# Performance work log

Hardware: AMD Instinct MI355X
Metric: run time of the kernel (lower is better)

## Reference

```python
import jax, jax.numpy as jnp
import numpy as np

N_NODES = 50000
N_EDGES = 800000
HIDDEN = 128
N_LAYERS = 3
MAX_Z = 1000
N_GRAPHS = 512
LN_EPS = 1e-5


def setup_inputs() -> dict:
    key = jax.random.key(0)
    ks = jax.random.split(key, 16)
    s = 0.05
    inp = {
        "z": jax.random.randint(ks[0], (N_NODES,), 0, MAX_Z),
        "edge_index": jax.random.randint(ks[1], (2, N_EDGES), 0, N_NODES),
        "batch": jnp.sort(jax.random.randint(ks[2], (N_NODES,), 0, N_GRAPHS)),
        "z_table": jax.random.normal(ks[3], (MAX_Z, HIDDEN), jnp.float32) * s,
        "W1": jax.random.normal(ks[4], (N_LAYERS, HIDDEN, HIDDEN), jnp.float32) * s,
        "b1": jnp.zeros((N_LAYERS, HIDDEN), jnp.float32),
        "W2": jax.random.normal(ks[5], (N_LAYERS, HIDDEN, HIDDEN), jnp.float32) * s,
        "b2": jnp.zeros((N_LAYERS, HIDDEN), jnp.float32),
        "ln_g": jnp.ones((N_LAYERS, HIDDEN), jnp.float32),
        "ln_b": jnp.zeros((N_LAYERS, HIDDEN), jnp.float32),
        "lin1_W": jax.random.normal(ks[6], (N_LAYERS * HIDDEN, HIDDEN), jnp.float32) * s,
        "lin1_b": jnp.zeros((HIDDEN,), jnp.float32),
        "lin2_W": jax.random.normal(ks[7], (HIDDEN, 1), jnp.float32) * s,
        "lin2_b": jnp.zeros((1,), jnp.float32),
    }
    return inp


def _layernorm(h, g, b):
    mu = jnp.mean(h, axis=-1, keepdims=True)
    var = jnp.mean((h - mu) ** 2, axis=-1, keepdims=True)
    return g * (h - mu) * jax.lax.rsqrt(var + LN_EPS) + b


def _gin_conv(x, src, dst, W1, b1, W2, b2, g, b):
    # sum-aggregate neighbor features, eps = 0 (train_eps=False)
    agg = jax.ops.segment_sum(x[src], dst, num_segments=N_NODES)
    h = x + agg
    h = jax.nn.relu(h @ W1 + b1)
    h = jax.nn.relu(h @ W2 + b2)
    return _layernorm(h, g, b)


def reference(z, edge_index, batch, z_table, W1, b1, W2, b2, ln_g, ln_b,
              lin1_W, lin1_b, lin2_W, lin2_b):
    src, dst = edge_index[0], edge_index[1]
    x = z_table[z]  # [N, H] z embedding (z is 1-D so no sum over dim 1)
    xs = []
    for l in range(N_LAYERS):
        x = _gin_conv(x, src, dst, W1[l], b1[l], W2[l], b2[l], ln_g[l], ln_b[l])
        xs.append(x)
    xcat = jnp.concatenate(xs, axis=1)  # JK concat [N, L*H]
    # global mean pool over graphs
    sums = jax.ops.segment_sum(xcat, batch, num_segments=N_GRAPHS)
    cnts = jax.ops.segment_sum(jnp.ones((N_NODES, 1), xcat.dtype), batch,
                               num_segments=N_GRAPHS)
    pooled = sums / jnp.maximum(cnts, 1.0)
    h = jax.nn.relu(pooled @ lin1_W + lin1_b)
    # dropout is identity in eval mode
    return h @ lin2_W + lin2_b  # [N_GRAPHS, 1]
```

## Files before the change

kernel.cpp:

```cpp
#include <hip/hip_runtime.h>
#include <hip/hip_bf16.h>

#define NN 50000
#define NE 800000
#define HD 128
#define NL 3
#define NG 512
#define LN_EPS 1e-5f
#define NXCD 8
#define NPX 6250

typedef unsigned short u16;
typedef unsigned int u32;
typedef __attribute__((ext_vector_type(8))) short short8;
typedef __attribute__((ext_vector_type(4))) float f32x4;

__device__ __forceinline__ u16 f2bf(float f){
  u32 x = __float_as_uint(f);
  u32 r = (x + 0x7fffu + ((x >> 16) & 1u)) >> 16;
  return (u16)r;
}
__device__ __forceinline__ float blo(u32 u){ return __uint_as_float(u << 16); }
__device__ __forceinline__ float bhi(u32 u){ return __uint_as_float(u & 0xffff0000u); }
__device__ __forceinline__ u32 pk2(float a, float b){ return (u32)f2bf(a) | ((u32)f2bf(b) << 16); }

__device__ __forceinline__ int lower_bound_dev(const int* a, int n, int v){
  int lo = 0, hi = n;
  while (lo < hi){ int m = (lo + hi) >> 1; if (a[m] < v) lo = m + 1; else hi = m; }
  return lo;
}

__global__ __launch_bounds__(256) void k_prep_w(const float* __restrict__ W1,
    const float* __restrict__ W2, u16* __restrict__ Wt){
  int t = blockIdx.x * 256 + threadIdx.x;
  if (t >= 6 * 128 * 128) return;
  int w = t >> 14, r = t & 16383, n = r >> 7, k = r & 127;
  int l = w >> 1;
  const float* Ws = (w & 1) ? (W2 + l * 16384) : (W1 + l * 16384);
  Wt[t] = f2bf(Ws[k * 128 + n]);
}

__global__ __launch_bounds__(256) void k_embed(const int* __restrict__ z,
    const float* __restrict__ tab, u16* __restrict__ xb){
  int gt = blockIdx.x * 256 + threadIdx.x;
  int node = gt >> 5, q = gt & 31;
  float4 v = *reinterpret_cast<const float4*>(tab + (size_t)z[node] * 128 + q * 4);
  uint2 p = { pk2(v.x, v.y), pk2(v.z, v.w) };
  *reinterpret_cast<uint2*>(xb + (size_t)node * 128 + q * 4) = p;
}

__global__ __launch_bounds__(256) void k_count(const int* __restrict__ dst,
    int* __restrict__ deg){
  int xcd = blockIdx.x & 7;
  int grp = blockIdx.x >> 3;
  int nlo = xcd * NPX, nhi = nlo + NPX;
  for (int e = grp * 256 + threadIdx.x; e < NE; e += 128 * 256){
    int d = dst[e];
    if (d >= nlo && d < nhi) atomicAdd(&deg[d], 1);
  }
}

__global__ __launch_bounds__(256) void k_scan1(const int* __restrict__ deg,
    int* __restrict__ part, int* __restrict__ bsum){
  int i = blockIdx.x * 256 + threadIdx.x;
  int v = (i < NN) ? deg[i] : 0;
  int lane = threadIdx.x & 63, wave = threadIdx.x >> 6;
  int s = v;
  for (int off = 1; off < 64; off <<= 1){ int n = __shfl_up(s, off); if (lane >= off) s += n; }
  __shared__ int wsums[4];
  if (lane == 63) wsums[wave] = s;
  __syncthreads();
  int add = 0;
  for (int w = 0; w < wave; ++w) add += wsums[w];
  int incl = s + add;
  if (i < NN) part[i] = incl - v;
  if (threadIdx.x == 255) bsum[blockIdx.x] = incl;
}

__global__ __launch_bounds__(256) void k_scan2(int* __restrict__ bsum, int nb){
  int tid = threadIdx.x;
  int v = (tid < nb) ? bsum[tid] : 0;
  int lane = tid & 63, wave = tid >> 6;
  int s = v;
  for (int off = 1; off < 64; off <<= 1){ int n = __shfl_up(s, off); if (lane >= off) s += n; }
  __shared__ int wsums[4];
  if (lane == 63) wsums[wave] = s;
  __syncthreads();
  int add = 0;
  for (int w = 0; w < wave; ++w) add += wsums[w];
  int incl = s + add;
  if (tid < nb) bsum[tid] = incl - v;
}

__global__ __launch_bounds__(256) void k_scan3(const int* __restrict__ part,
    const int* __restrict__ bsum, int* __restrict__ rowptr, int* __restrict__ cursor){
  int i = blockIdx.x * 256 + threadIdx.x;
  if (i < NN){ int r = part[i] + bsum[blockIdx.x]; rowptr[i] = r; cursor[i] = r; }
  if (i == 0) rowptr[NN] = NE;
}

__global__ __launch_bounds__(256) void k_fill(const int* __restrict__ src,
    const int* __restrict__ dst, int* __restrict__ cursor, u16* __restrict__ col){
  int xcd = blockIdx.x & 7;
  int grp = blockIdx.x >> 3;
  int nlo = xcd * NPX, nhi = nlo + NPX;
  for (int e = grp * 256 + threadIdx.x; e < NE; e += 128 * 256){
    int d = dst[e];
    if (d >= nlo && d < nhi){
      int p = atomicAdd(&cursor[d], 1);
      col[p] = (u16)src[e];
    }
  }
}

__global__ __launch_bounds__(256) void k_gather(const int* __restrict__ rowptr,
    const u16* __restrict__ col, const u16* __restrict__ xb, u16* __restrict__ hb){
  int wave = threadIdx.x >> 6, lane = threadIdx.x & 63;
  int node = blockIdx.x * 4 + wave;
  int q = lane >> 4, l4 = lane & 15;
  float a[8] = {0.f,0.f,0.f,0.f,0.f,0.f,0.f,0.f};
  float b[8] = {0.f,0.f,0.f,0.f,0.f,0.f,0.f,0.f};
  if (q == 0){
    uint4 s = *reinterpret_cast<const uint4*>(xb + (size_t)node * 128 + l4 * 8);
    a[0] = blo(s.x); a[1] = bhi(s.x); a[2] = blo(s.y); a[3] = bhi(s.y);
    a[4] = blo(s.z); a[5] = bhi(s.z); a[6] = blo(s.w); a[7] = bhi(s.w);
  }
  int lo = rowptr[node], hi = rowptr[node + 1];
  int e = lo + q;
  for (; e + 12 < hi; e += 16){
    int c0 = col[e], c1 = col[e + 4], c2 = col[e + 8], c3 = col[e + 12];
    uint4 v0 = *reinterpret_cast<const uint4*>(xb + (size_t)c0 * 128 + l4 * 8);
    uint4 v1 = *reinterpret_cast<const uint4*>(xb + (size_t)c1 * 128 + l4 * 8);
    uint4 v2 = *reinterpret_cast<const uint4*>(xb + (size_t)c2 * 128 + l4 * 8);
    uint4 v3 = *reinterpret_cast<const uint4*>(xb + (size_t)c3 * 128 + l4 * 8);
    a[0] += blo(v0.x); a[1] += bhi(v0.x); a[2] += blo(v0.y); a[3] += bhi(v0.y);
    a[4] += blo(v0.z); a[5] += bhi(v0.z); a[6] += blo(v0.w); a[7] += bhi(v0.w);
    b[0] += blo(v1.x); b[1] += bhi(v1.x); b[2] += blo(v1.y); b[3] += bhi(v1.y);
    b[4] += blo(v1.z); b[5] += bhi(v1.z); b[6] += blo(v1.w); b[7] += bhi(v1.w);
    a[0] += blo(v2.x); a[1] += bhi(v2.x); a[2] += blo(v2.y); a[3] += bhi(v2.y);
    a[4] += blo(v2.z); a[5] += bhi(v2.z); a[6] += blo(v2.w); a[7] += bhi(v2.w);
    b[0] += blo(v3.x); b[1] += bhi(v3.x); b[2] += blo(v3.y); b[3] += bhi(v3.y);
    b[4] += blo(v3.z); b[5] += bhi(v3.z); b[6] += blo(v3.w); b[7] += bhi(v3.w);
  }
  for (; e < hi; e += 4){
    int c0 = col[e];
    uint4 v0 = *reinterpret_cast<const uint4*>(xb + (size_t)c0 * 128 + l4 * 8);
    a[0] += blo(v0.x); a[1] += bhi(v0.x); a[2] += blo(v0.y); a[3] += bhi(v0.y);
    a[4] += blo(v0.z); a[5] += bhi(v0.z); a[6] += blo(v0.w); a[7] += bhi(v0.w);
  }
  #pragma unroll
  for (int j = 0; j < 8; ++j){
    a[j] += b[j];
    a[j] += __shfl_xor(a[j], 16);
    a[j] += __shfl_xor(a[j], 32);
  }
  if (q == 0){
    uint4 p = { pk2(a[0], a[1]), pk2(a[2], a[3]), pk2(a[4], a[5]), pk2(a[6], a[7]) };
    *reinterpret_cast<uint4*>(hb + (size_t)node * 128 + l4 * 8) = p;
  }
}

__global__ __launch_bounds__(256) void k_layer(const u16* __restrict__ A,
    const u16* __restrict__ Wt1, const u16* __restrict__ Wt2,
    const float* __restrict__ bias1, const float* __restrict__ bias2,
    const float* __restrict__ lng, const float* __restrict__ lnb,
    u16* __restrict__ Cout, const int* __restrict__ batch,
    float* __restrict__ pooled, int lsl){
  __shared__ u16 As[128 * 128];
  __shared__ int sb[128];
  int tid = threadIdx.x;
  int rb = blockIdx.x * 128;

  #pragma unroll
  for (int i = 0; i < 8; ++i){
    int u = tid + i * 256;
    int row = u >> 4, k8 = u & 15;
    int grow = rb + row;
    uint4 v = {0u, 0u, 0u, 0u};
    if (grow < NN) v = *reinterpret_cast<const uint4*>(A + (size_t)grow * 128 + k8 * 8);
    *reinterpret_cast<uint4*>(&As[row * 128 + (k8 ^ (row & 15)) * 8]) = v;
  }
  if (tid < 128){
    int grow = rb + tid;
    sb[tid] = (grow < NN) ? batch[grow] : -1;
  }
  __syncthreads();

  int wave = tid >> 6, lane = tid & 63;
  int lrow = lane & 15, kgrp = lane >> 4;
  f32x4 acc[2][8];
  #pragma unroll
  for (int rt = 0; rt < 2; ++rt)
    #pragma unroll
    for (int nt = 0; nt < 8; ++nt) acc[rt][nt] = (f32x4){0.f, 0.f, 0.f, 0.f};

  #pragma unroll
  for (int ks = 0; ks < 4; ++ks){
    int ch = ks * 4 + kgrp;
    short8 a0 = *reinterpret_cast<const short8*>(&As[(wave * 32 + lrow) * 128 + (ch ^ lrow) * 8]);
    short8 a1 = *reinterpret_cast<const short8*>(&As[(wave * 32 + 16 + lrow) * 128 + (ch ^ lrow) * 8]);
    #pragma unroll
    for (int nt = 0; nt < 8; ++nt){
      short8 b = *reinterpret_cast<const short8*>(Wt1 + (nt * 16 + lrow) * 128 + ch * 8);
      acc[0][nt] = __builtin_amdgcn_mfma_f32_16x16x32_bf16(a0, b, acc[0][nt], 0, 0, 0);
      acc[1][nt] = __builtin_amdgcn_mfma_f32_16x16x32_bf16(a1, b, acc[1][nt], 0, 0, 0);
    }
  }

  #pragma unroll
  for (int nt = 0; nt < 8; ++nt){
    float bv = __ldg(bias1 + nt * 16 + lrow);
    #pragma unroll
    for (int rt = 0; rt < 2; ++rt)
      #pragma unroll
      for (int j = 0; j < 4; ++j)
        acc[rt][nt][j] = fmaxf(acc[rt][nt][j] + bv, 0.f);
  }

  __syncthreads();
  #pragma unroll
  for (int rt = 0; rt < 2; ++rt)
    #pragma unroll
    for (int j = 0; j < 4; ++j){
      int row = wave * 32 + rt * 16 + kgrp * 4 + j;
      #pragma unroll
      for (int nt = 0; nt < 8; ++nt){
        int col = nt * 16 + lrow;
        int ch = (col >> 3) ^ (row & 15);
        As[row * 128 + ch * 8 + (col & 7)] = f2bf(acc[rt][nt][j]);
      }
    }
  __syncthreads();

  #pragma unroll
  for (int rt = 0; rt < 2; ++rt)
    #pragma unroll
    for (int nt = 0; nt < 8; ++nt) acc[rt][nt] = (f32x4){0.f, 0.f, 0.f, 0.f};

  #pragma unroll
  for (int ks = 0; ks < 4; ++ks){
    int ch = ks * 4 + kgrp;
    short8 a0 = *reinterpret_cast<const short8*>(&As[(wave * 32 + lrow) * 128 + (ch ^ lrow) * 8]);
    short8 a1 = *reinterpret_cast<const short8*>(&As[(wave * 32 + 16 + lrow) * 128 + (ch ^ lrow) * 8]);
    #pragma unroll
    for (int nt = 0; nt < 8; ++nt){
      short8 b = *reinterpret_cast<const short8*>(Wt2 + (nt * 16 + lrow) * 128 + ch * 8);
      acc[0][nt] = __builtin_amdgcn_mfma_f32_16x16x32_bf16(a0, b, acc[0][nt], 0, 0, 0);
      acc[1][nt] = __builtin_amdgcn_mfma_f32_16x16x32_bf16(a1, b, acc[1][nt], 0, 0, 0);
    }
  }

  float gv[8], lbv[8];
  #pragma unroll
  for (int nt = 0; nt < 8; ++nt){
    int gcol = nt * 16 + lrow;
    float bv = __ldg(bias2 + gcol);
    gv[nt] = __ldg(lng + gcol); lbv[nt] = __ldg(lnb + gcol);
    #pragma unroll
    for (int rt = 0; rt < 2; ++rt)
      #pragma unroll
      for (int j = 0; j < 4; ++j)
        acc[rt][nt][j] = fmaxf(acc[rt][nt][j] + bv, 0.f);
  }
  #pragma unroll
  for (int rt = 0; rt < 2; ++rt)
    #pragma unroll
    for (int j = 0; j < 4; ++j){
      float s = 0.f, sq = 0.f;
      #pragma unroll
      for (int nt = 0; nt < 8; ++nt){ float v = acc[rt][nt][j]; s += v; sq += v * v; }
      #pragma unroll
      for (int off = 1; off < 16; off <<= 1){
        s += __shfl_xor(s, off); sq += __shfl_xor(sq, off);
      }
      float mu = s * (1.f / 128.f);
      float var = sq * (1.f / 128.f) - mu * mu;
      float rstd = rsqrtf(var + LN_EPS);
      #pragma unroll
      for (int nt = 0; nt < 8; ++nt)
        acc[rt][nt][j] = gv[nt] * (acc[rt][nt][j] - mu) * rstd + lbv[nt];
    }

  #pragma unroll
  for (int rt = 0; rt < 2; ++rt){
    int rbase = rb + wave * 32 + rt * 16 + kgrp * 4;
    #pragma unroll
    for (int nt = 0; nt < 8; ++nt){
      int gcol = nt * 16 + lrow;
      #pragma unroll
      for (int j = 0; j < 4; ++j){
        int grow = rbase + j;
        if (grow < NN) Cout[(size_t)grow * 128 + gcol] = f2bf(acc[rt][nt][j]);
      }
    }
  }

  __syncthreads();
  #pragma unroll
  for (int rt = 0; rt < 2; ++rt)
    #pragma unroll
    for (int j = 0; j < 4; ++j){
      int row = wave * 32 + rt * 16 + kgrp * 4 + j;
      #pragma unroll
      for (int nt = 0; nt < 8; ++nt){
        int col = nt * 16 + lrow;
        int ch = (col >> 3) ^ (row & 15);
        As[row * 128 + ch * 8 + (col & 7)] = f2bf(acc[rt][nt][j]);
      }
    }
  __syncthreads();
  int f = tid & 127, half = tid >> 7;
  int cur = -1; float sum = 0.f;
  for (int r = half * 64; r < half * 64 + 64; ++r){
    int g = sb[r];
    if (g != cur){
      if (cur >= 0) atomicAdd(&pooled[(size_t)cur * 384 + lsl * 128 + f], sum);
      cur = g; sum = 0.f;
    }
    if (g >= 0){
      int ch = (f >> 3) ^ (r & 15);
      sum += blo((u32)As[r * 128 + ch * 8 + (f & 7)]);
    }
  }
  if (cur >= 0) atomicAdd(&pooled[(size_t)cur * 384 + lsl * 128 + f], sum);
}

__global__ __launch_bounds__(128) void k_final(const float* __restrict__ pooled,
    const int* __restrict__ batch, const float* __restrict__ W1,
    const float* __restrict__ b1, const float* __restrict__ W2,
    const float* __restrict__ b2, float* __restrict__ out){
  int g = blockIdx.x, f = threadIdx.x;
  int lo = lower_bound_dev(batch, NN, g);
  int hi = lower_bound_dev(batch, NN, g + 1);
  float scale = 1.f / fmaxf((float)(hi - lo), 1.f);
  __shared__ float p[384];
  for (int k = f; k < 384; k += 128) p[k] = pooled[(size_t)g * 384 + k] * scale;
  __syncthreads();
  float acc = __ldg(b1 + f);
  for (int k = 0; k < 384; ++k) acc += p[k] * __ldg(W1 + k * 128 + f);
  float hval = fmaxf(acc, 0.f);
  float v = hval * __ldg(W2 + f);
  for (int off = 32; off; off >>= 1) v += __shfl_xor(v, off);
  __shared__ float red[2];
  int lane = f & 63, wave = f >> 6;
  if (lane == 0) red[wave] = v;
  __syncthreads();
  if (f == 0) out[g] = red[0] + red[1] + __ldg(b2);
}

extern "C" void kernel_launch(void* const* d_in, const int* in_sizes, int n_in,
                              void* d_out, int out_size, void* d_ws, size_t ws_size,
                              hipStream_t stream){
  const int*   z     = (const int*)d_in[0];
  const int*   ei    = (const int*)d_in[1];
  const int*   batch = (const int*)d_in[2];
  const float* ztab  = (const float*)d_in[3];
  const float* W1    = (const float*)d_in[4];
  const float* b1    = (const float*)d_in[5];
  const float* W2    = (const float*)d_in[6];
  const float* b2    = (const float*)d_in[7];
  const float* lng   = (const float*)d_in[8];
  const float* lnb   = (const float*)d_in[9];
  const float* l1W   = (const float*)d_in[10];
  const float* l1b   = (const float*)d_in[11];
  const float* l2W   = (const float*)d_in[12];
  const float* l2b   = (const float*)d_in[13];
  float* out = (float*)d_out;

  char* wsb = (char*)d_ws;
  size_t off = 0;
  auto alloc = [&](size_t bytes){ void* p = wsb + off; off += (bytes + 255) & ~(size_t)255; return p; };
  u16*   xbf    = (u16*)alloc((size_t)NN * 128 * 2);
  u16*   hbf    = (u16*)alloc((size_t)NN * 128 * 2);
  u16*   Wt     = (u16*)alloc((size_t)6 * 128 * 128 * 2);
  int*   deg    = (int*)alloc((size_t)NN * 4);
  float* pooled = (float*)alloc((size_t)NG * 384 * 4);
  int*   part   = (int*)alloc((size_t)NN * 4);
  int*   bsum   = (int*)alloc((size_t)256 * 4);
  int*   rowptr = (int*)alloc((size_t)(NN + 1) * 4);
  int*   cursor = (int*)alloc((size_t)NN * 4);
  u16*   col    = (u16*)alloc((size_t)NE * 2);

  const int* srcv = ei;
  const int* dstv = ei + NE;

  size_t zero_bytes = ((size_t)NN * 4 + 255 & ~(size_t)255) + (size_t)NG * 384 * 4;
  hipMemsetAsync(deg, 0, zero_bytes, stream);
  k_prep_w<<<(6 * 128 * 128 + 255) / 256, 256, 0, stream>>>(W1, W2, Wt);
  k_embed<<<NN * 32 / 256, 256, 0, stream>>>(z, ztab, xbf);
  k_count<<<1024, 256, 0, stream>>>(dstv, deg);
  int nb = (NN + 255) / 256;
  k_scan1<<<nb, 256, 0, stream>>>(deg, part, bsum);
  k_scan2<<<1, 256, 0, stream>>>(bsum, nb);
  k_scan3<<<nb, 256, 0, stream>>>(part, bsum, rowptr, cursor);
  k_fill<<<1024, 256, 0, stream>>>(srcv, dstv, cursor, col);

  int gb = (NN + 127) / 128;
  for (int l = 0; l < NL; ++l){
    k_gather<<<NN / 4, 256, 0, stream>>>(rowptr, col, xbf, hbf);
    k_layer<<<gb, 256, 0, stream>>>(hbf,
        Wt + (size_t)(l * 2 + 0) * 16384, Wt + (size_t)(l * 2 + 1) * 16384,
        b1 + l * 128, b2 + l * 128, lng + l * 128, lnb + l * 128, xbf,
        batch, pooled, l);
  }
  k_final<<<NG, 128, 0, stream>>>(pooled, batch, l1W, l1b, l2W, l2b, out);
}
```

Before: 448.1 us.

## Halve k_layer row tile, drop intermediate syncs, coalesce output via LDS

After: 419.3 us. 1.07x faster.

```diff
diff --git a/kernel.cpp b/kernel.cpp
--- a/kernel.cpp
+++ b/kernel.cpp
@@ -166,13 +166,13 @@
     const float* __restrict__ lng, const float* __restrict__ lnb,
     u16* __restrict__ Cout, const int* __restrict__ batch,
     float* __restrict__ pooled, int lsl){
-  __shared__ u16 As[128 * 128];
-  __shared__ int sb[128];
+  __shared__ u16 As[64 * 128];
+  __shared__ int sb[64];
   int tid = threadIdx.x;
-  int rb = blockIdx.x * 128;
-
-  #pragma unroll
-  for (int i = 0; i < 8; ++i){
+  int rb = blockIdx.x * 64;
+
+  #pragma unroll
+  for (int i = 0; i < 4; ++i){
     int u = tid + i * 256;
     int row = u >> 4, k8 = u & 15;
     int grow = rb + row;
@@ -180,7 +180,7 @@
     if (grow < NN) v = *reinterpret_cast<const uint4*>(A + (size_t)grow * 128 + k8 * 8);
     *reinterpret_cast<uint4*>(&As[row * 128 + (k8 ^ (row & 15)) * 8]) = v;
   }
-  if (tid < 128){
+  if (tid < 64){
     int grow = rb + tid;
     sb[tid] = (grow < NN) ? batch[grow] : -1;
   }
@@ -188,65 +188,44 @@
 
   int wave = tid >> 6, lane = tid & 63;
   int lrow = lane & 15, kgrp = lane >> 4;
-  f32x4 acc[2][8];
-  #pragma unroll
-  for (int rt = 0; rt < 2; ++rt)
-    #pragma unroll
-    for (int nt = 0; nt < 8; ++nt) acc[rt][nt] = (f32x4){0.f, 0.f, 0.f, 0.f};
-
+  int wr = wave * 16;
+  f32x4 acc[8];
+
+  #pragma unroll
+  for (int nt = 0; nt < 8; ++nt) acc[nt] = (f32x4){0.f, 0.f, 0.f, 0.f};
   #pragma unroll
   for (int ks = 0; ks < 4; ++ks){
     int ch = ks * 4 + kgrp;
-    short8 a0 = *reinterpret_cast<const short8*>(&As[(wave * 32 + lrow) * 128 + (ch ^ lrow) * 8]);
-    short8 a1 = *reinterpret_cast<const short8*>(&As[(wave * 32 + 16 + lrow) * 128 + (ch ^ lrow) * 8]);
+    short8 a0 = *reinterpret_cast<const short8*>(&As[(wr + lrow) * 128 + (ch ^ lrow) * 8]);
     #pragma unroll
     for (int nt = 0; nt < 8; ++nt){
       short8 b = *reinterpret_cast<const short8*>(Wt1 + (nt * 16 + lrow) * 128 + ch * 8);
-      acc[0][nt] = __builtin_amdgcn_mfma_f32_16x16x32_bf16(a0, b, acc[0][nt], 0, 0, 0);
-      acc[1][nt] = __builtin_amdgcn_mfma_f32_16x16x32_bf16(a1, b, acc[1][nt], 0, 0, 0);
-    }
-  }
-
+      acc[nt] = __builtin_amdgcn_mfma_f32_16x16x32_bf16(a0, b, acc[nt], 0, 0, 0);
+    }
+  }
   #pragma unroll
   for (int nt = 0; nt < 8; ++nt){
     float bv = __ldg(bias1 + nt * 16 + lrow);
     #pragma unroll
-    for (int rt = 0; rt < 2; ++rt)
-      #pragma unroll
-      for (int j = 0; j < 4; ++j)
-        acc[rt][nt][j] = fmaxf(acc[rt][nt][j] + bv, 0.f);
-  }
-
-  __syncthreads();
-  #pragma unroll
-  for (int rt = 0; rt < 2; ++rt)
-    #pragma unroll
     for (int j = 0; j < 4; ++j){
-      int row = wave * 32 + rt * 16 + kgrp * 4 + j;
-      #pragma unroll
-      for (int nt = 0; nt < 8; ++nt){
-        int col = nt * 16 + lrow;
-        int ch = (col >> 3) ^ (row & 15);
-        As[row * 128 + ch * 8 + (col & 7)] = f2bf(acc[rt][nt][j]);
-      }
-    }
-  __syncthreads();
-
-  #pragma unroll
-  for (int rt = 0; rt < 2; ++rt)
-    #pragma unroll
-    for (int nt = 0; nt < 8; ++nt) acc[rt][nt] = (f32x4){0.f, 0.f, 0.f, 0.f};
-
+      float v = fmaxf(acc[nt][j] + bv, 0.f);
+      int row = wr + kgrp * 4 + j;
+      int colc = nt * 16 + lrow;
+      int ch = (colc >> 3) ^ (row & 15);
+      As[row * 128 + ch * 8 + (colc & 7)] = f2bf(v);
+    }
+  }
+
+  #pragma unroll
+  for (int nt = 0; nt < 8; ++nt) acc[nt] = (f32x4){0.f, 0.f, 0.f, 0.f};
   #pragma unroll
   for (int ks = 0; ks < 4; ++ks){
     int ch = ks * 4 + kgrp;
-    short8 a0 = *reinterpret_cast<const short8*>(&As[(wave * 32 + lrow) * 128 + (ch ^ lrow) * 8]);
-    short8 a1 = *reinterpret_cast<const short8*>(&As[(wave * 32 + 16 + lrow) * 128 + (ch ^ lrow) * 8]);
+    short8 a0 = *reinterpret_cast<const short8*>(&As[(wr + lrow) * 128 + (ch ^ lrow) * 8]);
     #pragma unroll
     for (int nt = 0; nt < 8; ++nt){
       short8 b = *reinterpret_cast<const short8*>(Wt2 + (nt * 16 + lrow) * 128 + ch * 8);
-      acc[0][nt] = __builtin_amdgcn_mfma_f32_16x16x32_bf16(a0, b, acc[0][nt], 0, 0, 0);
-      acc[1][nt] = __builtin_amdgcn_mfma_f32_16x16x32_bf16(a1, b, acc[1][nt], 0, 0, 0);
+      acc[nt] = __builtin_amdgcn_mfma_f32_16x16x32_bf16(a0, b, acc[nt], 0, 0, 0);
     }
   }
 
@@ -257,69 +236,66 @@
     float bv = __ldg(bias2 + gcol);
     gv[nt] = __ldg(lng + gcol); lbv[nt] = __ldg(lnb + gcol);
     #pragma unroll
-    for (int rt = 0; rt < 2; ++rt)
-      #pragma unroll
-      for (int j = 0; j < 4; ++j)
-        acc[rt][nt][j] = fmaxf(acc[rt][nt][j] + bv, 0.f);
-  }
-  #pragma unroll
-  for (int rt = 0; rt < 2; ++rt)
+    for (int j = 0; j < 4; ++j)
+      acc[nt][j] = fmaxf(acc[nt][j] + bv, 0.f);
+  }
+  #pragma unroll
+  for (int j = 0; j < 4; ++j){
+    float s = 0.f, sq = 0.f;
+    #pragma unroll
+    for (int nt = 0; nt < 8; ++nt){ float v = acc[nt][j]; s += v; sq += v * v; }
+    #pragma unroll
+    for (int off = 1; off < 16; off <<= 1){
+      s += __shfl_xor(s, off); sq += __shfl_xor(sq, off);
+    }
+    float mu = s * (1.f / 128.f);
+    float var = sq * (1.f / 128.f) - mu * mu;
+    float rstd = rsqrtf(var + LN_EPS);
+    #pragma unroll
+    for (int nt = 0; nt < 8; ++nt)
+      acc[nt][j] = gv[nt] * (acc[nt][j] - mu) * rstd + lbv[nt];
+  }
+
+  #pragma unroll
+  for (int nt = 0; nt < 8; ++nt)
     #pragma unroll
     for (int j = 0; j < 4; ++j){
-      float s = 0.f, sq = 0.f;
-      #pragma unroll
-      for (int nt = 0; nt < 8; ++nt){ float v = acc[rt][nt][j]; s += v; sq += v * v; }
-      #pragma unroll
-      for (int off = 1; off < 16; off <<= 1){
-        s += __shfl_xor(s, off); sq += __shfl_xor(sq, off);
-      }
-      float mu = s * (1.f / 128.f);
-      float var = sq * (1.f / 128.f) - mu * mu;
-      float rstd = rsqrtf(var + LN_EPS);
-      #pragma unroll
-      for (int nt = 0; nt < 8; ++nt)
-        acc[rt][nt][j] = gv[nt] * (acc[rt][nt][j] - mu) * rstd + lbv[nt];
-    }
-
-  #pragma unroll
-  for (int rt = 0; rt < 2; ++rt){
-    int rbase = rb + wave * 32 + rt * 16 + kgrp * 4;
-    #pragma unroll
-    for (int nt = 0; nt < 8; ++nt){
-      int gcol = nt * 16 + lrow;
-      #pragma unroll
-      for (int j = 0; j < 4; ++j){
-        int grow = rbase + j;
-        if (grow < NN) Cout[(size_t)grow * 128 + gcol] = f2bf(acc[rt][nt][j]);
-      }
-    }
-  }
-
-  __syncthreads();
-  #pragma unroll
-  for (int rt = 0; rt < 2; ++rt)
-    #pragma unroll
-    for (int j = 0; j < 4; ++j){
-      int row = wave * 32 + rt * 16 + kgrp * 4 + j;
-      #pragma unroll
-      for (int nt = 0; nt < 8; ++nt){
-        int col = nt * 16 + lrow;
-        int ch = (col >> 3) ^ (row & 15);
-        As[row * 128 + ch * 8 + (col & 7)] = f2bf(acc[rt][nt][j]);
-      }
-    }
-  __syncthreads();
+      int row = wr + kgrp * 4 + j;
+      int colc = nt * 16 + lrow;
+      int ch = (colc >> 3) ^ (row & 15);
+      As[row * 128 + ch * 8 + (colc & 7)] = f2bf(acc[nt][j]);
+    }
+  __syncthreads();
+
+  #pragma unroll
+  for (int i = 0; i < 4; ++i){
+    int u = tid + i * 256;
+    int row = u >> 4, k8 = u & 15;
+    int grow = rb + row;
+    if (grow < NN){
+      uint4 v = *reinterpret_cast<const uint4*>(&As[row * 128 + (k8 ^ (row & 15)) * 8]);
+      *reinterpret_cast<uint4*>(Cout + (size_t)grow * 128 + k8 * 8) = v;
+    }
+  }
+
   int f = tid & 127, half = tid >> 7;
   int cur = -1; float sum = 0.f;
-  for (int r = half * 64; r < half * 64 + 64; ++r){
-    int g = sb[r];
-    if (g != cur){
-      if (cur >= 0) atomicAdd(&pooled[(size_t)cur * 384 + lsl * 128 + f], sum);
-      cur = g; sum = 0.f;
-    }
-    if (g >= 0){
+  for (int rr = half * 32; rr < half * 32 + 32; rr += 8){
+    float v[8]; int gg[8];
+    #pragma unroll
+    for (int k = 0; k < 8; ++k){
+      int r = rr + k;
       int ch = (f >> 3) ^ (r & 15);
-      sum += blo((u32)As[r * 128 + ch * 8 + (f & 7)]);
+      v[k] = blo((u32)As[r * 128 + ch * 8 + (f & 7)]);
+      gg[k] = sb[r];
+    }
+    #pragma unroll
+    for (int k = 0; k < 8; ++k){
+      if (gg[k] != cur){
+        if (cur >= 0) atomicAdd(&pooled[(size_t)cur * 384 + lsl * 128 + f], sum);
+        cur = gg[k]; sum = 0.f;
+      }
+      if (gg[k] >= 0) sum += v[k];
     }
   }
   if (cur >= 0) atomicAdd(&pooled[(size_t)cur * 384 + lsl * 128 + f], sum);
@@ -395,7 +371,7 @@
   k_scan3<<<nb, 256, 0, stream>>>(part, bsum, rowptr, cursor);
   k_fill<<<1024, 256, 0, stream>>>(srcv, dstv, cursor, col);
 
-  int gb = (NN + 127) / 128;
+  int gb = (NN + 63) / 64;
   for (int l = 0; l < NL; ++l){
     k_gather<<<NN / 4, 256, 0, stream>>>(rowptr, col, xbf, hbf);
     k_layer<<<gb, 256, 0, stream>>>(hbf,
```
